# Optimization experiments

Measured on AMD Instinct MI355X. Metric: run time of the kernel, lower is better.

Reference implementation:

```python
import math
import jax, jax.numpy as jnp
import numpy as np

N_HEADS = 16
D_EMBED = 1024
D_HEAD = D_EMBED // N_HEADS  # 64; only used for the scale factor (see bug note)
B, N = 4, 4096


def setup_inputs() -> dict:
    key = jax.random.key(0)
    k1, k2, k3, k4, k5 = jax.random.split(key, 5)
    return {
        "x": jax.random.normal(k1, (B, N, D_EMBED), dtype=jnp.float32),
        "W_qkv_w": jax.random.normal(k2, (3 * D_EMBED, D_EMBED), dtype=jnp.float32) * 0.02,
        "W_qkv_b": jax.random.normal(k3, (3 * D_EMBED,), dtype=jnp.float32) * 0.02,
        "W_o_w": jax.random.normal(k4, (D_EMBED, D_EMBED), dtype=jnp.float32) * 0.02,
        "W_o_b": jax.random.normal(k5, (D_EMBED,), dtype=jnp.float32) * 0.02,
    }


def reference(x, W_qkv_w, W_qkv_b, W_o_w, W_o_b):
    # Faithful to source, including its bugs:
    #  - q/k/v are never actually reshaped to heads (the .view().transpose()
    #    results are discarded), so attention runs over full d_embed vectors
    #    with scale 1/sqrt(d_head).
    #  - the final transpose(1,2).reshape scrambles the output layout.
    b, n, d = x.shape
    qkv = x @ W_qkv_w.T + W_qkv_b                      # [b, n, 3d]
    q, k, v = jnp.split(qkv, 3, axis=-1)               # each [b, n, d]
    scores = jnp.einsum("bqd,bkd->bqk", q, k)          # [b, n, n]
    causal = jnp.triu(jnp.ones((n, n), dtype=bool), 1)
    scale = jnp.float32(1.0 / math.sqrt(D_HEAD))
    scores = jnp.where(causal, -jnp.inf, scores * scale)
    weights = jax.nn.softmax(scores, axis=-1)
    out = jnp.einsum("bqk,bkd->bqd", weights, v)       # [b, n, d]
    out = jnp.swapaxes(out, 1, 2).reshape(b, n, d)     # scramble (as in source)
    return out @ W_o_w.T + W_o_b
```

## Files before the change

### kernel.cpp

```cpp
#include <hip/hip_runtime.h>
#include <math.h>

#define TB 256

typedef __attribute__((ext_vector_type(8))) short short8_t;
typedef __attribute__((ext_vector_type(4))) float f32x4;

__device__ __forceinline__ ushort f2bf(float f) {
    uint u = __float_as_uint(f);
    return (ushort)((u + 0x7FFFu + ((u >> 16) & 1u)) >> 16);
}

__device__ __forceinline__ void gload_lds16(const void* g, void* l) {
    __builtin_amdgcn_global_load_lds(
        (const __attribute__((address_space(1))) void*)g,
        (__attribute__((address_space(3))) void*)l, 16, 0, 0);
}

template<int CONV, int EPI, bool TRI, bool KLIM, bool REVX, bool SPLITK>
__global__ __launch_bounds__(TB)
void gemm_bf16(const void* __restrict__ Av, int lda,
               const ushort* __restrict__ B, int ldb,
               const float* __restrict__ bias,
               void* __restrict__ Cv, int ldc,
               int K, float alpha, int off)
{
    constexpr int BM = 128, BN = 128, BK = 32;
    const int m0 = blockIdx.y * BM;
    const int nb = REVX ? (gridDim.x - 1 - blockIdx.x) : blockIdx.x;
    const int n0 = nb * BN;
    if (TRI && n0 > m0 + off + BM - 1) return;

    const int tid = threadIdx.x;
    const int lane = tid & 63;
    const int wid = tid >> 6;
    const int wr = wid >> 1, wc = wid & 1;

    __shared__ __align__(16) ushort As[3][BM * BK];
    __shared__ __align__(16) ushort Bs[3][BN * BK];

    f32x4 acc[4][4];
    const f32x4 zero = {0.f, 0.f, 0.f, 0.f};
    #pragma unroll
    for (int mi = 0; mi < 4; mi++)
        #pragma unroll
        for (int ni = 0; ni < 4; ni++) acc[mi][ni] = zero;

    const int klim = KLIM ? (n0 + off + BN) : K;
    const int kend = klim < K ? klim : K;
    const int ntf = kend / BK;
    int t0 = 0, t1 = ntf;
    if (SPLITK) {
        const int half = (ntf + 1) >> 1;
        if (blockIdx.z == 0) t1 = half; else t0 = half;
    }
    const int ntl = t1 - t0;

    auto STAGE = [&](int t, int s) {
        const int k0 = t * BK;
        if (CONV) {
            const float* Af = (const float*)Av;
            #pragma unroll
            for (int h = 0; h < 2; h++) {
                const int q = tid + h * TB;
                const int row = q >> 2;
                const int kp = (q & 3) * 8;
                const float* src = &Af[(size_t)(m0 + row) * lda + k0 + kp];
                float4 u0 = *(const float4*)src;
                float4 u1 = *(const float4*)(src + 4);
                short8_t sv;
                sv[0] = (short)f2bf(u0.x); sv[1] = (short)f2bf(u0.y);
                sv[2] = (short)f2bf(u0.z); sv[3] = (short)f2bf(u0.w);
                sv[4] = (short)f2bf(u1.x); sv[5] = (short)f2bf(u1.y);
                sv[6] = (short)f2bf(u1.z); sv[7] = (short)f2bf(u1.w);
                *(short8_t*)&As[s][row * BK + kp] = sv;
            }
        } else {
            const ushort* Ab = (const ushort*)Av;
            const int c = wid * 2;
            const int row0 = c * 16 + (lane >> 2);
            const int row1 = row0 + 16;
            const int kh = (lane & 3) * 8;
            gload_lds16(&Ab[(size_t)(m0 + row0) * lda + k0 + kh],
                        (char*)&As[s][0] + c * 1024);
            gload_lds16(&Ab[(size_t)(m0 + row1) * lda + k0 + kh],
                        (char*)&As[s][0] + (c + 1) * 1024);
        }
        const int c = wid * 2;
        const int row0 = c * 16 + (lane >> 2);
        const int row1 = row0 + 16;
        const int kh = (lane & 3) * 8;
        gload_lds16(&B[(size_t)(n0 + row0) * ldb + k0 + kh],
                    (char*)&Bs[s][0] + c * 1024);
        gload_lds16(&B[(size_t)(n0 + row1) * ldb + k0 + kh],
                    (char*)&Bs[s][0] + (c + 1) * 1024);
    };

    auto wait_pipe = [&]() {
        if constexpr (CONV != 0) asm volatile("s_waitcnt vmcnt(2)" ::: "memory");
        else                     asm volatile("s_waitcnt vmcnt(4)" ::: "memory");
    };
    auto wait_zero = [&]() { asm volatile("s_waitcnt vmcnt(0)" ::: "memory"); };
    auto wait_lgkm = [&]() {
        if constexpr (CONV != 0) asm volatile("s_waitcnt lgkmcnt(0)" ::: "memory");
    };

    STAGE(t0, 0);
    if (ntl > 1) { STAGE(t0 + 1, 1); wait_pipe(); }
    else         { wait_zero(); }
    wait_lgkm();
    __builtin_amdgcn_s_barrier();

    const int frow = lane & 15;
    const int kh8  = (lane >> 4) * 8;

    for (int u = 0; u < ntl; u++) {
        const int cur = u % 3;
        if (u + 2 < ntl) STAGE(t0 + u + 2, (u + 2) % 3);

        short8_t a[4], b[4];
        #pragma unroll
        for (int mi = 0; mi < 4; mi++)
            a[mi] = *(const short8_t*)&As[cur][(wr * 64 + mi * 16 + frow) * BK + kh8];
        #pragma unroll
        for (int ni = 0; ni < 4; ni++)
            b[ni] = *(const short8_t*)&Bs[cur][(wc * 64 + ni * 16 + frow) * BK + kh8];
        #pragma unroll
        for (int mi = 0; mi < 4; mi++)
            #pragma unroll
            for (int ni = 0; ni < 4; ni++)
                acc[mi][ni] = __builtin_amdgcn_mfma_f32_16x16x32_bf16(
                    a[mi], b[ni], acc[mi][ni], 0, 0, 0);

        if (u + 1 < ntl) {
            if (u + 2 < ntl) wait_pipe();
            else             wait_zero();
            wait_lgkm();
            __builtin_amdgcn_s_barrier();
        }
    }

    void* Czv = Cv;
    if (SPLITK)
        Czv = (void*)((float*)Cv + (size_t)blockIdx.z * 1024 * 4096);
    const int col = lane & 15;
    const int rb  = (lane >> 4) * 4;
    #pragma unroll
    for (int mi = 0; mi < 4; mi++) {
        #pragma unroll
        for (int ni = 0; ni < 4; ni++) {
            const int r = m0 + wr * 64 + mi * 16 + rb;
            const int c = n0 + wc * 64 + ni * 16 + col;
            f32x4 v = acc[mi][ni];
            if (EPI == 0) {
                ushort* C = (ushort*)Czv;
                const float bz = bias[c];
                #pragma unroll
                for (int t = 0; t < 4; t++)
                    C[(size_t)(r + t) * ldc + c] = f2bf(v[t] + bz);
            } else if (EPI == 1) {
                float* C = (float*)Czv;
                #pragma unroll
                for (int t = 0; t < 4; t++)
                    C[(size_t)(r + t) * ldc + c] = v[t] * alpha;
            } else {
                float* C = (float*)Czv;
                const float bz = bias[c];
                #pragma unroll
                for (int t = 0; t < 4; t++)
                    C[(size_t)(r + t) * ldc + c] = v[t] + bz;
            }
        }
    }
}

__global__ __launch_bounds__(TB)
void conv_f32_bf16(const float* __restrict__ in, ushort* __restrict__ out, int n4)
{
    for (int i = blockIdx.x * TB + threadIdx.x; i < n4; i += gridDim.x * TB) {
        float4 v = ((const float4*)in)[i];
        ushort4 o;
        o.x = f2bf(v.x); o.y = f2bf(v.y); o.z = f2bf(v.z); o.w = f2bf(v.w);
        ((ushort4*)out)[i] = o;
    }
}

__global__ __launch_bounds__(TB)
void reduce_pair_bf16(const float* __restrict__ a, const float* __restrict__ b,
                      ushort* __restrict__ o, int n4)
{
    for (int i = blockIdx.x * TB + threadIdx.x; i < n4; i += gridDim.x * TB) {
        float4 x = ((const float4*)a)[i];
        float4 y = ((const float4*)b)[i];
        ushort4 z;
        z.x = f2bf(x.x + y.x); z.y = f2bf(x.y + y.y);
        z.z = f2bf(x.z + y.z); z.w = f2bf(x.w + y.w);
        ((ushort4*)o)[i] = z;
    }
}

__global__ __launch_bounds__(TB)
void transposeV(const ushort* __restrict__ V, int ldv, ushort* __restrict__ Vt)
{
    __shared__ ushort Ls[64][65];
    const int n0 = blockIdx.x * 64, d0 = blockIdx.y * 64;
    const int t = threadIdx.x;
    #pragma unroll
    for (int p = 0; p < 4; p++) {
        const int row = p * 16 + (t >> 4);
        const int c4 = (t & 15) * 4;
        ushort4 v = *(const ushort4*)&V[(size_t)(n0 + row) * ldv + d0 + c4];
        Ls[row][c4 + 0] = v.x; Ls[row][c4 + 1] = v.y;
        Ls[row][c4 + 2] = v.z; Ls[row][c4 + 3] = v.w;
    }
    __syncthreads();
    #pragma unroll
    for (int p = 0; p < 4; p++) {
        const int d = p * 16 + (t >> 4);
        const int n4 = (t & 15) * 4;
        ushort4 o;
        o.x = Ls[n4 + 0][d]; o.y = Ls[n4 + 1][d];
        o.z = Ls[n4 + 2][d]; o.w = Ls[n4 + 3][d];
        *(ushort4*)&Vt[(size_t)(d0 + d) * 4096 + n0 + n4] = o;
    }
}

__global__ __launch_bounds__(TB)
void softmax_prefix(float* __restrict__ Sp, ushort* __restrict__ Pp, int r0)
{
    const int local = blockIdx.x;
    const int r = r0 + local;
    const int pe = ((r >> 7) << 7) + 128;
    float* p = Sp + (size_t)local * 4096;
    ushort* q = Pp + (size_t)local * 4096;
    const int t = threadIdx.x;
    const int wv = t >> 6, ln = t & 63;
    __shared__ float red[4];

    float lm = -INFINITY;
    for (int k4 = t * 4; k4 < pe; k4 += 1024) {
        float4 v = *(const float4*)&p[k4];
        lm = (k4 + 0 <= r) ? fmaxf(lm, v.x) : lm;
        lm = (k4 + 1 <= r) ? fmaxf(lm, v.y) : lm;
        lm = (k4 + 2 <= r) ? fmaxf(lm, v.z) : lm;
        lm = (k4 + 3 <= r) ? fmaxf(lm, v.w) : lm;
    }
    #pragma unroll
    for (int m = 1; m < 64; m <<= 1) lm = fmaxf(lm, __shfl_xor(lm, m, 64));
    if (ln == 0) red[wv] = lm;
    __syncthreads();
    const float mx = fmaxf(fmaxf(red[0], red[1]), fmaxf(red[2], red[3]));
    __syncthreads();

    float ls = 0.f;
    for (int k4 = t * 4; k4 < pe; k4 += 1024) {
        float4 v = *(const float4*)&p[k4];
        float4 e;
        e.x = (k4 + 0 <= r) ? __expf(v.x - mx) : 0.f;
        e.y = (k4 + 1 <= r) ? __expf(v.y - mx) : 0.f;
        e.z = (k4 + 2 <= r) ? __expf(v.z - mx) : 0.f;
        e.w = (k4 + 3 <= r) ? __expf(v.w - mx) : 0.f;
        ls += e.x + e.y + e.z + e.w;
        *(float4*)&p[k4] = e;
    }
    #pragma unroll
    for (int m = 1; m < 64; m <<= 1) ls += __shfl_xor(ls, m, 64);
    if (ln == 0) red[wv] = ls;
    __syncthreads();
    const float inv = 1.0f / (red[0] + red[1] + red[2] + red[3]);
    for (int k4 = t * 4; k4 < pe; k4 += 1024) {
        float4 e = *(const float4*)&p[k4];
        ushort4 o;
        o.x = f2bf(e.x * inv); o.y = f2bf(e.y * inv);
        o.z = f2bf(e.z * inv); o.w = f2bf(e.w * inv);
        *(ushort4*)&q[k4] = o;
    }
}

extern "C" void kernel_launch(void* const* d_in, const int* in_sizes, int n_in,
                              void* d_out, int out_size, void* d_ws, size_t ws_size,
                              hipStream_t stream)
{
    const float* x    = (const float*)d_in[0];
    const float* Wqkv = (const float*)d_in[1];
    const float* bqkv = (const float*)d_in[2];
    const float* Wo   = (const float*)d_in[3];
    const float* bo   = (const float*)d_in[4];
    float* out = (float*)d_out;

    ushort* Wq    = (ushort*)d_ws;
    ushort* Wob   = Wq    + (size_t)3072 * 1024;
    ushort* qkvb  = Wob   + (size_t)1024 * 1024;
    ushort* Vtb   = qkvb  + (size_t)4096 * 3072;
    ushort* Tall  = Vtb   + (size_t)1024 * 4096;
    ushort* Pch   = Tall  + (size_t)4 * 1024 * 4096;
    float*  Sch   = (float*)(Pch + (size_t)4096 * 4096);
    float*  Tpart = Sch + (size_t)4096 * 4096;

    dim3 blk(TB);

    conv_f32_bf16<<<256, blk, 0, stream>>>(Wqkv, Wq,  3072 * 1024 / 4);
    conv_f32_bf16<<<128, blk, 0, stream>>>(Wo,   Wob, 1024 * 1024 / 4);

    for (int b = 0; b < 4; b++) {
        const float* xb = x + (size_t)b * 4096 * 1024;
        gemm_bf16<1, 0, false, false, false, false><<<dim3(24, 32), blk, 0, stream>>>(
            xb, 1024, Wq, 1024, bqkv, qkvb, 3072, 1024, 1.f, 0);

        transposeV<<<dim3(64, 16), blk, 0, stream>>>(qkvb + 2048, 3072, Vtb);

        gemm_bf16<0, 1, true, false, false, false><<<dim3(32, 32), blk, 0, stream>>>(
            qkvb, 3072, qkvb + 1024, 3072, nullptr, Sch, 4096, 1024, 0.125f, 0);

        softmax_prefix<<<dim3(4096), blk, 0, stream>>>(Sch, Pch, 0);

        gemm_bf16<0, 1, false, true, true, true><<<dim3(32, 8, 2), blk, 0, stream>>>(
            Vtb, 4096, Pch, 4096, nullptr, Tpart, 4096, 4096, 1.f, 0);

        reduce_pair_bf16<<<1024, blk, 0, stream>>>(
            Tpart, Tpart + (size_t)1024 * 4096,
            Tall + (size_t)b * 1024 * 4096, 1024 * 4096 / 4);
    }

    gemm_bf16<0, 3, false, false, false, false><<<dim3(8, 128), blk, 0, stream>>>(
        Tall, 1024, Wob, 1024, bo, out, 1024, 1024, 1.f, 0);
}
```

Baseline: 852.8 us.

## Pre-convert x to bf16, add BM=64 tiles, XCD swizzle and reversed rows

```diff
diff --git a/kernel.cpp b/kernel.cpp
--- a/kernel.cpp
+++ b/kernel.cpp
@@ -17,34 +17,46 @@
         (__attribute__((address_space(3))) void*)l, 16, 0, 0);
 }
 
-template<int CONV, int EPI, bool TRI, bool KLIM, bool REVX, bool SPLITK>
-__global__ __launch_bounds__(TB)
-void gemm_bf16(const void* __restrict__ Av, int lda,
+template<int BM, int EPI, bool TRI, bool KLIM, bool REVX, bool REVY,
+         bool SPLITK, bool XCD>
+__global__ __launch_bounds__(TB)
+void gemm_bf16(const ushort* __restrict__ A, int lda,
                const ushort* __restrict__ B, int ldb,
                const float* __restrict__ bias,
                void* __restrict__ Cv, int ldc,
                int K, float alpha, int off)
 {
-    constexpr int BM = 128, BN = 128, BK = 32;
-    const int m0 = blockIdx.y * BM;
-    const int nb = REVX ? (gridDim.x - 1 - blockIdx.x) : blockIdx.x;
+    constexpr int BN = 128, BK = 32;
+    constexpr int NI = (BM == 128) ? 4 : 2;
+
+    int bx = blockIdx.x, by = blockIdx.y;
+    if (XCD) {
+        const int gx = gridDim.x;
+        const int nwg = gx * gridDim.y;
+        const int lin = by * gx + bx;
+        const int swz = (lin & 7) * (nwg >> 3) + (lin >> 3);
+        bx = swz % gx; by = swz / gx;
+    }
+    const int m0 = (REVY ? (gridDim.y - 1 - by) : by) * BM;
+    const int nb = REVX ? (gridDim.x - 1 - bx) : bx;
     const int n0 = nb * BN;
     if (TRI && n0 > m0 + off + BM - 1) return;
 
     const int tid = threadIdx.x;
     const int lane = tid & 63;
     const int wid = tid >> 6;
-    const int wr = wid >> 1, wc = wid & 1;
+    const int arow = (BM == 128) ? (wid >> 1) * 64 : 0;
+    const int bcol = (BM == 128) ? (wid & 1) * 64 : wid * 32;
 
     __shared__ __align__(16) ushort As[3][BM * BK];
     __shared__ __align__(16) ushort Bs[3][BN * BK];
 
-    f32x4 acc[4][4];
+    f32x4 acc[4][NI];
     const f32x4 zero = {0.f, 0.f, 0.f, 0.f};
     #pragma unroll
     for (int mi = 0; mi < 4; mi++)
         #pragma unroll
-        for (int ni = 0; ni < 4; ni++) acc[mi][ni] = zero;
+        for (int ni = 0; ni < NI; ni++) acc[mi][ni] = zero;
 
     const int klim = KLIM ? (n0 + off + BN) : K;
     const int kend = klim < K ? klim : K;
@@ -58,57 +70,35 @@
 
     auto STAGE = [&](int t, int s) {
         const int k0 = t * BK;
-        if (CONV) {
-            const float* Af = (const float*)Av;
-            #pragma unroll
-            for (int h = 0; h < 2; h++) {
-                const int q = tid + h * TB;
-                const int row = q >> 2;
-                const int kp = (q & 3) * 8;
-                const float* src = &Af[(size_t)(m0 + row) * lda + k0 + kp];
-                float4 u0 = *(const float4*)src;
-                float4 u1 = *(const float4*)(src + 4);
-                short8_t sv;
-                sv[0] = (short)f2bf(u0.x); sv[1] = (short)f2bf(u0.y);
-                sv[2] = (short)f2bf(u0.z); sv[3] = (short)f2bf(u0.w);
-                sv[4] = (short)f2bf(u1.x); sv[5] = (short)f2bf(u1.y);
-                sv[6] = (short)f2bf(u1.z); sv[7] = (short)f2bf(u1.w);
-                *(short8_t*)&As[s][row * BK + kp] = sv;
-            }
+        const int kh = (lane & 3) * 8;
+        const int rsub = lane >> 2;
+        if constexpr (BM == 128) {
+            const int c = wid * 2;
+            gload_lds16(&A[(size_t)(m0 + c * 16 + rsub) * lda + k0 + kh],
+                        (char*)&As[s][0] + c * 1024);
+            gload_lds16(&A[(size_t)(m0 + c * 16 + 16 + rsub) * lda + k0 + kh],
+                        (char*)&As[s][0] + (c + 1) * 1024);
         } else {
-            const ushort* Ab = (const ushort*)Av;
-            const int c = wid * 2;
-            const int row0 = c * 16 + (lane >> 2);
-            const int row1 = row0 + 16;
-            const int kh = (lane & 3) * 8;
-            gload_lds16(&Ab[(size_t)(m0 + row0) * lda + k0 + kh],
+            const int c = wid;
+            gload_lds16(&A[(size_t)(m0 + c * 16 + rsub) * lda + k0 + kh],
                         (char*)&As[s][0] + c * 1024);
-            gload_lds16(&Ab[(size_t)(m0 + row1) * lda + k0 + kh],
-                        (char*)&As[s][0] + (c + 1) * 1024);
         }
-        const int c = wid * 2;
-        const int row0 = c * 16 + (lane >> 2);
-        const int row1 = row0 + 16;
-        const int kh = (lane & 3) * 8;
-        gload_lds16(&B[(size_t)(n0 + row0) * ldb + k0 + kh],
-                    (char*)&Bs[s][0] + c * 1024);
-        gload_lds16(&B[(size_t)(n0 + row1) * ldb + k0 + kh],
-                    (char*)&Bs[s][0] + (c + 1) * 1024);
+        const int cb = wid * 2;
+        gload_lds16(&B[(size_t)(n0 + cb * 16 + rsub) * ldb + k0 + kh],
+                    (char*)&Bs[s][0] + cb * 1024);
+        gload_lds16(&B[(size_t)(n0 + cb * 16 + 16 + rsub) * ldb + k0 + kh],
+                    (char*)&Bs[s][0] + (cb + 1) * 1024);
     };
 
     auto wait_pipe = [&]() {
-        if constexpr (CONV != 0) asm volatile("s_waitcnt vmcnt(2)" ::: "memory");
-        else                     asm volatile("s_waitcnt vmcnt(4)" ::: "memory");
+        if constexpr (BM == 128) asm volatile("s_waitcnt vmcnt(4)" ::: "memory");
+        else                     asm volatile("s_waitcnt vmcnt(3)" ::: "memory");
     };
     auto wait_zero = [&]() { asm volatile("s_waitcnt vmcnt(0)" ::: "memory"); };
-    auto wait_lgkm = [&]() {
-        if constexpr (CONV != 0) asm volatile("s_waitcnt lgkmcnt(0)" ::: "memory");
-    };
 
     STAGE(t0, 0);
     if (ntl > 1) { STAGE(t0 + 1, 1); wait_pipe(); }
     else         { wait_zero(); }
-    wait_lgkm();
     __builtin_amdgcn_s_barrier();
 
     const int frow = lane & 15;
@@ -118,24 +108,23 @@
         const int cur = u % 3;
         if (u + 2 < ntl) STAGE(t0 + u + 2, (u + 2) % 3);
 
-        short8_t a[4], b[4];
+        short8_t a[4], b[NI];
         #pragma unroll
         for (int mi = 0; mi < 4; mi++)
-            a[mi] = *(const short8_t*)&As[cur][(wr * 64 + mi * 16 + frow) * BK + kh8];
-        #pragma unroll
-        for (int ni = 0; ni < 4; ni++)
-            b[ni] = *(const short8_t*)&Bs[cur][(wc * 64 + ni * 16 + frow) * BK + kh8];
+            a[mi] = *(const short8_t*)&As[cur][(arow + mi * 16 + frow) * BK + kh8];
+        #pragma unroll
+        for (int ni = 0; ni < NI; ni++)
+            b[ni] = *(const short8_t*)&Bs[cur][(bcol + ni * 16 + frow) * BK + kh8];
         #pragma unroll
         for (int mi = 0; mi < 4; mi++)
             #pragma unroll
-            for (int ni = 0; ni < 4; ni++)
+            for (int ni = 0; ni < NI; ni++)
                 acc[mi][ni] = __builtin_amdgcn_mfma_f32_16x16x32_bf16(
                     a[mi], b[ni], acc[mi][ni], 0, 0, 0);
 
         if (u + 1 < ntl) {
             if (u + 2 < ntl) wait_pipe();
             else             wait_zero();
-            wait_lgkm();
             __builtin_amdgcn_s_barrier();
         }
     }
@@ -148,9 +137,9 @@
     #pragma unroll
     for (int mi = 0; mi < 4; mi++) {
         #pragma unroll
-        for (int ni = 0; ni < 4; ni++) {
-            const int r = m0 + wr * 64 + mi * 16 + rb;
-            const int c = n0 + wc * 64 + ni * 16 + col;
+        for (int ni = 0; ni < NI; ni++) {
+            const int r = m0 + arow + mi * 16 + rb;
+            const int c = n0 + bcol + ni * 16 + col;
             f32x4 v = acc[mi][ni];
             if (EPI == 0) {
                 ushort* C = (ushort*)Czv;
@@ -296,7 +285,7 @@
     ushort* Pch   = Tall  + (size_t)4 * 1024 * 4096;
     float*  Sch   = (float*)(Pch + (size_t)4096 * 4096);
     float*  Tpart = Sch + (size_t)4096 * 4096;
-
+    ushort* xscr  = (ushort*)Tpart;
     dim3 blk(TB);
 
     conv_f32_bf16<<<256, blk, 0, stream>>>(Wqkv, Wq,  3072 * 1024 / 4);
@@ -304,17 +293,23 @@
 
     for (int b = 0; b < 4; b++) {
         const float* xb = x + (size_t)b * 4096 * 1024;
-        gemm_bf16<1, 0, false, false, false, false><<<dim3(24, 32), blk, 0, stream>>>(
-            xb, 1024, Wq, 1024, bqkv, qkvb, 3072, 1024, 1.f, 0);
+
+        conv_f32_bf16<<<1024, blk, 0, stream>>>(xb, xscr, 4096 * 1024 / 4);
+
+        gemm_bf16<128, 0, false, false, false, false, false, true>
+            <<<dim3(24, 32), blk, 0, stream>>>(
+            xscr, 1024, Wq, 1024, bqkv, qkvb, 3072, 1024, 1.f, 0);
 
         transposeV<<<dim3(64, 16), blk, 0, stream>>>(qkvb + 2048, 3072, Vtb);
 
-        gemm_bf16<0, 1, true, false, false, false><<<dim3(32, 32), blk, 0, stream>>>(
+        gemm_bf16<64, 1, true, false, false, true, false, false>
+            <<<dim3(32, 64), blk, 0, stream>>>(
             qkvb, 3072, qkvb + 1024, 3072, nullptr, Sch, 4096, 1024, 0.125f, 0);
 
         softmax_prefix<<<dim3(4096), blk, 0, stream>>>(Sch, Pch, 0);
 
-        gemm_bf16<0, 1, false, true, true, true><<<dim3(32, 8, 2), blk, 0, stream>>>(
+        gemm_bf16<64, 1, false, true, true, false, true, false>
+            <<<dim3(32, 16, 2), blk, 0, stream>>>(
             Vtb, 4096, Pch, 4096, nullptr, Tpart, 4096, 4096, 1.f, 0);
 
         reduce_pair_bf16<<<1024, blk, 0, stream>>>(
@@ -322,6 +317,7 @@
             Tall + (size_t)b * 1024 * 4096, 1024 * 4096 / 4);
     }
 
-    gemm_bf16<0, 3, false, false, false, false><<<dim3(8, 128), blk, 0, stream>>>(
+    gemm_bf16<128, 3, false, false, false, false, false, true>
+        <<<dim3(8, 128), blk, 0, stream>>>(
         Tall, 1024, Wob, 1024, bo, out, 1024, 1024, 1.f, 0);
 }
```

After: 811.8 us. 4.8% less time.
